# Optimization experiments

Hardware: AMD Instinct MI355X
Metric: run time of the kernel (lower is better)

## Reference

```python
import jax, jax.numpy as jnp
import numpy as np
from jax import lax

EPS = 1e-8


def setup_inputs() -> dict:
    key = jax.random.key(0)
    k1, k2, k3, k4 = jax.random.split(key, 4)
    B, C_in, C_out, K, S, H, W = 16, 64, 64, 3, 512, 256, 256
    x = jax.random.normal(k1, (B, C_in, H, W), dtype=jnp.float32)
    style = jax.random.normal(k2, (B, S), dtype=jnp.float32)
    # kaiming_normal fan_in linear: std = 1/sqrt(fan_in)
    mod_weight = jax.random.normal(k3, (C_in, S), dtype=jnp.float32) / np.sqrt(S)
    mod_bias = jnp.ones((C_in,), dtype=jnp.float32)  # init.constant_(bias, 1.0)
    weight = jax.random.normal(k4, (1, C_out, C_in, K, K), dtype=jnp.float32) / np.sqrt(C_in * K * K)
    return {"x": x, "style": style, "mod_weight": mod_weight,
            "mod_bias": mod_bias, "weight": weight}


def reference(x, style, mod_weight, mod_bias, weight):
    B, C, H, W = x.shape
    _, O, _, K, _ = weight.shape
    pad = K // 2
    # modulation: Linear(style) -> (B, C_in), broadcast over (O, kh, kw)
    s = style @ mod_weight.T + mod_bias                      # (B, C)
    w = weight * s[:, None, :, None, None]                   # (B, O, C, K, K)
    # demodulate
    demod = lax.rsqrt(jnp.sum(w * w, axis=(2, 3, 4), keepdims=True) + EPS)
    w = w * demod
    # grouped conv with groups = batch (per-sample weights)
    w = w.reshape(B * O, C, K, K)
    xg = x.reshape(1, B * C, H, W)
    out = lax.conv_general_dilated(
        xg, w,
        window_strides=(1, 1),
        padding=[(pad, pad), (pad, pad)],
        dimension_numbers=("NCHW", "OIHW", "NCHW"),
        feature_group_count=B,
    )
    return out.reshape(B, O, H, W)
```

## Files before the change

kernel.cpp:

```cpp
#include <hip/hip_runtime.h>

typedef _Float16 v8h __attribute__((ext_vector_type(8)));
typedef _Float16 v2h __attribute__((ext_vector_type(2)));
typedef float    v4f __attribute__((ext_vector_type(4)));
typedef unsigned int u32;

__global__ void style_kernel(const float* __restrict__ style,
                             const float* __restrict__ mw,
                             const float* __restrict__ mb,
                             float* __restrict__ s_out) {
    const int b = blockIdx.x;
    const int t = threadIdx.x;
    const int c = t >> 2, q = t & 3;
    const float* st = style + b * 512 + q * 128;
    const float* w  = mw + c * 512 + q * 128;
    float acc = 0.f;
    #pragma unroll 8
    for (int i = 0; i < 128; ++i) acc += st[i] * w[i];
    acc += __shfl_xor(acc, 1);
    acc += __shfl_xor(acc, 2);
    if (q == 0) s_out[b * 64 + c] = acc + mb[c];
}

__global__ void wprep_kernel(const float* __restrict__ weight,
                             const float* __restrict__ s,
                             _Float16* __restrict__ wA) {
    const int blk = blockIdx.x;
    const int b = blk >> 6, o = blk & 63;
    const int lane = threadIdx.x;
    const float* wo = weight + o * 576;
    const float* sb = s + b * 64;
    float vals[9];
    float sum = 0.f;
    #pragma unroll
    for (int k = 0; k < 9; ++k) {
        int e = lane + k * 64;
        int c = e / 9;
        float v = wo[e] * sb[c];
        vals[k] = v;
        sum += v * v;
    }
    #pragma unroll
    for (int off = 32; off; off >>= 1) sum += __shfl_xor(sum, off);
    const float demod = 1.f / sqrtf(sum + 1e-8f);
    #pragma unroll
    for (int k = 0; k < 9; ++k) {
        int e = lane + k * 64;
        int c = e / 9, tap = e - c * 9;
        int ks = c >> 5, lg = (c >> 3) & 3, j = c & 7;
        int dst = (((b * 9 + tap) * 8 + ks * 4 + (o >> 4)) * 64 + lg * 16 + (o & 15)) * 8 + j;
        wA[dst] = (_Float16)(vals[k] * demod);
    }
}

__global__ __launch_bounds__(256)
void xprep_kernel(const float* __restrict__ x, _Float16* __restrict__ xh) {
    __shared__ u32 lt[32 * 257];
    const int tid = threadIdx.x;
    const int h = blockIdx.x;
    const int b = blockIdx.y;

    const float* xr = x + ((size_t)b << 22) + (h << 8) + tid;
    float va[64];
    #pragma unroll
    for (int c = 0; c < 64; ++c)
        va[c] = __builtin_nontemporal_load(&xr[(size_t)c << 16]);
    #pragma unroll
    for (int cp = 0; cp < 32; ++cp) {
        union { v2h h2; u32 u; } pk;
        pk.h2[0] = (_Float16)va[2 * cp];
        pk.h2[1] = (_Float16)va[2 * cp + 1];
        lt[cp * 257 + tid] = pk.u;
    }

    if (tid < 5) {
        const int idx = blockIdx.x * 5 + tid;
        if (idx < 1028) {
            int row, col;
            if (idx < 258)        { row = 0;             col = idx; }
            else if (idx < 516)   { row = 257;           col = idx - 258; }
            else if (idx < 772)   { row = idx - 516 + 1; col = 0; }
            else                  { row = idx - 772 + 1; col = 257; }
            v8h z = {};
            _Float16* p = xh + (size_t)b * (258 * 258 * 64)
                             + (size_t)(row * 258 + col) * 64;
            #pragma unroll
            for (int g = 0; g < 8; ++g)
                *reinterpret_cast<v8h*>(p + g * 8) = z;
        }
    }
    __syncthreads();

    _Float16* rowb = xh + ((size_t)(b * 258 + h + 1) * 258 + 1) * 64;
    #pragma unroll
    for (int k = 0; k < 8; ++k) {
        const int G = (k << 8) + tid;
        const int pix = G >> 3, g = G & 7;
        union { u32 u[4]; v8h h8; } as_;
        #pragma unroll
        for (int jj = 0; jj < 4; ++jj)
            as_.u[jj] = lt[(4 * g + jj) * 257 + pix];
        *reinterpret_cast<v8h*>(rowb + (size_t)G * 8) = as_.h8;
    }
}

__global__ __launch_bounds__(256, 2)
void conv_kernel(const _Float16* __restrict__ xh,
                 const _Float16* __restrict__ wA,
                 float* __restrict__ out) {
    __shared__ __align__(16) _Float16 lds[612 * 64];

    const int tid = threadIdx.x;
    const int fid = blockIdx.x + (blockIdx.y << 3) + (blockIdx.z << 7);
    const int vid = ((fid & 7) << 8) + (fid >> 3);
    const int tx = vid & 7;
    const int ty = (vid >> 3) & 15;
    const int b  = vid >> 7;

    const int h0 = ty << 4;
    const int w0 = tx << 5;

    const int lane = tid & 63, wv = tid >> 6;
    const _Float16* xhb = xh + (size_t)b * (258 * 258 * 64);

    #pragma unroll
    for (int i = 0; i < 11; ++i) {
        const int k = wv + (i << 2);
        const int g0 = (k < 43) ? ((k << 6) < 2656 ? (k << 6) : 2656) : 0;
        const int A = g0 + lane;
        const int pix = A >> 3, g = A & 7;
        const int ph = pix / 34, pw = pix - ph * 34;
        const _Float16* src = xhb + (size_t)((h0 + ph) * 258 + (w0 + pw)) * 64
                                  + ((g ^ (pix & 7)) << 3);
        __builtin_amdgcn_global_load_lds(
            (const __attribute__((address_space(1))) void*)src,
            (__attribute__((address_space(3))) void*)(lds + (size_t)A * 8),
            16, 0, 0);
    }
    #pragma unroll
    for (int i = 0; i < 9; ++i) {
        const int k = wv + (i << 2);
        const int g0 = 2720 + ((k < 34) ? (k << 6) : 0);
        const int A = g0 + lane;
        const int pix = A >> 3, g = A & 7;
        const int ph = pix / 34, pw = pix - ph * 34;
        const _Float16* src = xhb + (size_t)((h0 + ph) * 258 + (w0 + pw)) * 64
                                  + ((g ^ (pix & 7)) << 3);
        __builtin_amdgcn_global_load_lds(
            (const __attribute__((address_space(1))) void*)src,
            (__attribute__((address_space(3))) void*)(lds + (size_t)A * 8),
            16, 0, 0);
    }

    const int n = lane & 15, lg = lane >> 4;
    const _Float16* wab = wA + (size_t)b * (9 * 8 * 64 * 8);

    v4f acc[4][2][2];

    asm volatile("s_waitcnt vmcnt(9)" ::: "memory");
    __builtin_amdgcn_s_barrier();
    __builtin_amdgcn_sched_barrier(0);

    #pragma unroll
    for (int ot = 0; ot < 4; ++ot)
        #pragma unroll
        for (int hf = 0; hf < 2; ++hf)
            #pragma unroll
            for (int rq = 0; rq < 2; ++rq)
                acc[ot][hf][rq] = (v4f)0.f;

    #pragma unroll
    for (int t = 0; t < 9; ++t) {
        const int dh = t / 3, dw = t - dh * 3;
        v8h a[4][2];
        #pragma unroll
        for (int ot = 0; ot < 4; ++ot)
            #pragma unroll
            for (int ks = 0; ks < 2; ++ks)
                a[ot][ks] = *reinterpret_cast<const v8h*>(
                    wab + ((size_t)((t * 8 + ks * 4 + ot) * 64 + lane)) * 8);
        #pragma unroll
        for (int rq = 0; rq < 2; ++rq) {
            const int R = wv + (rq << 2);
            #pragma unroll
            for (int hf = 0; hf < 2; ++hf) {
                const int pix = (R + dh) * 34 + n + (hf << 4) + dw;
                const char* pb = reinterpret_cast<const char*>(lds) + pix * 128;
                const int px7 = pix & 7;
                #pragma unroll
                for (int ks = 0; ks < 2; ++ks) {
                    v8h bf = *reinterpret_cast<const v8h*>(
                        pb + ((((ks << 2) + lg) ^ px7) << 4));
                    #pragma unroll
                    for (int ot = 0; ot < 4; ++ot)
                        acc[ot][hf][rq] = __builtin_amdgcn_mfma_f32_16x16x32_f16(
                            a[ot][ks], bf, acc[ot][hf][rq], 0, 0, 0);
                }
            }
        }
    }

    asm volatile("s_waitcnt vmcnt(0)" ::: "memory");
    __builtin_amdgcn_s_barrier();
    __builtin_amdgcn_sched_barrier(0);

    #pragma unroll
    for (int ot = 0; ot < 4; ++ot) {
        #pragma unroll
        for (int rq = 0; rq < 2; ++rq) {
            const int h = h0 + wv + (rq << 2);
            #pragma unroll
            for (int reg = 0; reg < 4; ++reg) {
                const int o = (ot << 4) + (lg << 2) + reg;
                float* op = out + (((size_t)(b * 64 + o)) << 16) + (h << 8) + w0 + n;
                __builtin_nontemporal_store(acc[ot][0][rq][reg], op);
                __builtin_nontemporal_store(acc[ot][1][rq][reg], op + 16);
            }
        }
    }

    #pragma unroll
    for (int ot = 0; ot < 4; ++ot)
        #pragma unroll
        for (int hf = 0; hf < 2; ++hf)
            #pragma unroll
            for (int rq = 0; rq < 2; ++rq)
                acc[ot][hf][rq] = (v4f)0.f;

    #pragma unroll
    for (int t = 0; t < 9; ++t) {
        const int dh = t / 3, dw = t - dh * 3;
        v8h a[4][2];
        #pragma unroll
        for (int ot = 0; ot < 4; ++ot)
            #pragma unroll
            for (int ks = 0; ks < 2; ++ks)
                a[ot][ks] = *reinterpret_cast<const v8h*>(
                    wab + ((size_t)((t * 8 + ks * 4 + ot) * 64 + lane)) * 8);
        #pragma unroll
        for (int rq = 0; rq < 2; ++rq) {
            const int R = wv + 8 + (rq << 2);
            #pragma unroll
            for (int hf = 0; hf < 2; ++hf) {
                const int pix = (R + dh) * 34 + n + (hf << 4) + dw;
                const char* pb = reinterpret_cast<const char*>(lds) + pix * 128;
                const int px7 = pix & 7;
                #pragma unroll
                for (int ks = 0; ks < 2; ++ks) {
                    v8h bf = *reinterpret_cast<const v8h*>(
                        pb + ((((ks << 2) + lg) ^ px7) << 4));
                    #pragma unroll
                    for (int ot = 0; ot < 4; ++ot)
                        acc[ot][hf][rq] = __builtin_amdgcn_mfma_f32_16x16x32_f16(
                            a[ot][ks], bf, acc[ot][hf][rq], 0, 0, 0);
                }
            }
        }
    }

    #pragma unroll
    for (int ot = 0; ot < 4; ++ot) {
        #pragma unroll
        for (int rq = 0; rq < 2; ++rq) {
            const int h = h0 + wv + 8 + (rq << 2);
            #pragma unroll
            for (int reg = 0; reg < 4; ++reg) {
                const int o = (ot << 4) + (lg << 2) + reg;
                float* op = out + (((size_t)(b * 64 + o)) << 16) + (h << 8) + w0 + n;
                __builtin_nontemporal_store(acc[ot][0][rq][reg], op);
                __builtin_nontemporal_store(acc[ot][1][rq][reg], op + 16);
            }
        }
    }
}

extern "C" void kernel_launch(void* const* d_in, const int* in_sizes, int n_in,
                              void* d_out, int out_size, void* d_ws, size_t ws_size,
                              hipStream_t stream) {
    const float* x      = (const float*)d_in[0];
    const float* style  = (const float*)d_in[1];
    const float* mw     = (const float*)d_in[2];
    const float* mb     = (const float*)d_in[3];
    const float* weight = (const float*)d_in[4];
    float* out = (float*)d_out;

    float*    s_ws = (float*)d_ws;
    _Float16* wA   = (_Float16*)((char*)d_ws + 4096);
    _Float16* xh   = (_Float16*)((char*)d_ws + 2u * 1024u * 1024u);

    style_kernel<<<16, 256, 0, stream>>>(style, mw, mb, s_ws);
    wprep_kernel<<<1024, 64, 0, stream>>>(weight, s_ws, wA);
    xprep_kernel<<<dim3(256, 16), 256, 0, stream>>>(x, xh);
    conv_kernel<<<dim3(8, 16, 16), 256, 0, stream>>>(xh, wA, out);
}
```

Baseline: 188.7 us.

## Shrink conv LDS tile to a 12-row ring buffer and raise occupancy to three blocks

The conv kernel now stages only the first 12 halo rows plus part of the rest into LDS, then refills the first rows with the remaining 6 rows after the first half's compute. The second half indexes rows modulo 12. This cuts LDS per block from 612 to 408 pixel slots, so the launch bound is raised to allow three resident blocks per CU. The trade-off is an extra barrier and a refill load in the middle of the kernel, plus a tighter register budget that could cause spills.

```diff
diff --git a/kernel.cpp b/kernel.cpp
--- a/kernel.cpp
+++ b/kernel.cpp
@@ -104,11 +104,11 @@
     }
 }
 
-__global__ __launch_bounds__(256, 2)
+__global__ __launch_bounds__(256, 3)
 void conv_kernel(const _Float16* __restrict__ xh,
                  const _Float16* __restrict__ wA,
                  float* __restrict__ out) {
-    __shared__ __align__(16) _Float16 lds[612 * 64];
+    __shared__ __align__(16) _Float16 lds[408 * 64];
 
     const int tid = threadIdx.x;
     const int fid = blockIdx.x + (blockIdx.y << 3) + (blockIdx.z << 7);
@@ -123,33 +123,28 @@
     const int lane = tid & 63, wv = tid >> 6;
     const _Float16* xhb = xh + (size_t)b * (258 * 258 * 64);
 
-    #pragma unroll
-    for (int i = 0; i < 11; ++i) {
-        const int k = wv + (i << 2);
-        const int g0 = (k < 43) ? ((k << 6) < 2656 ? (k << 6) : 2656) : 0;
-        const int A = g0 + lane;
-        const int pix = A >> 3, g = A & 7;
+    auto stage = [&](int Ag, int Ad) {
+        const int pix = Ag >> 3, g = Ag & 7;
         const int ph = pix / 34, pw = pix - ph * 34;
         const _Float16* src = xhb + (size_t)((h0 + ph) * 258 + (w0 + pw)) * 64
                                   + ((g ^ (pix & 7)) << 3);
         __builtin_amdgcn_global_load_lds(
             (const __attribute__((address_space(1))) void*)src,
-            (__attribute__((address_space(3))) void*)(lds + (size_t)A * 8),
+            (__attribute__((address_space(3))) void*)(lds + (size_t)Ad * 8),
             16, 0, 0);
-    }
-    #pragma unroll
-    for (int i = 0; i < 9; ++i) {
+    };
+
+    #pragma unroll
+    for (int i = 0; i < 11; ++i) {
         const int k = wv + (i << 2);
-        const int g0 = 2720 + ((k < 34) ? (k << 6) : 0);
-        const int A = g0 + lane;
-        const int pix = A >> 3, g = A & 7;
-        const int ph = pix / 34, pw = pix - ph * 34;
-        const _Float16* src = xhb + (size_t)((h0 + ph) * 258 + (w0 + pw)) * 64
-                                  + ((g ^ (pix & 7)) << 3);
-        __builtin_amdgcn_global_load_lds(
-            (const __attribute__((address_space(1))) void*)src,
-            (__attribute__((address_space(3))) void*)(lds + (size_t)A * 8),
-            16, 0, 0);
+        const int g0 = min(k << 6, 2656);
+        stage(g0 + lane, g0 + lane);
+    }
+    #pragma unroll
+    for (int i = 0; i < 3; ++i) {
+        const int k = wv + (i << 2);
+        const int g0 = 2720 + min(k << 6, 480);
+        stage(g0 + lane, g0 + lane);
     }
 
     const int n = lane & 15, lg = lane >> 4;
@@ -157,7 +152,7 @@
 
     v4f acc[4][2][2];
 
-    asm volatile("s_waitcnt vmcnt(9)" ::: "memory");
+    asm volatile("s_waitcnt vmcnt(3)" ::: "memory");
     __builtin_amdgcn_s_barrier();
     __builtin_amdgcn_sched_barrier(0);
 
@@ -200,6 +195,15 @@
         }
     }
 
+    __builtin_amdgcn_s_barrier();
+    __builtin_amdgcn_sched_barrier(0);
+
+    #pragma unroll
+    for (int i = 0; i < 7; ++i) {
+        const int k = wv + (i << 2);
+        const int g0 = min(k << 6, 1568);
+        stage(3264 + g0 + lane, g0 + lane);
+    }
     asm volatile("s_waitcnt vmcnt(0)" ::: "memory");
     __builtin_amdgcn_s_barrier();
     __builtin_amdgcn_sched_barrier(0);
@@ -239,12 +243,13 @@
                     wab + ((size_t)((t * 8 + ks * 4 + ot) * 64 + lane)) * 8);
         #pragma unroll
         for (int rq = 0; rq < 2; ++rq) {
-            const int R = wv + 8 + (rq << 2);
+            const int row = wv + 8 + (rq << 2) + dh;
+            const int srow = (row < 12) ? row : row - 12;
             #pragma unroll
             for (int hf = 0; hf < 2; ++hf) {
-                const int pix = (R + dh) * 34 + n + (hf << 4) + dw;
-                const char* pb = reinterpret_cast<const char*>(lds) + pix * 128;
-                const int px7 = pix & 7;
+                const int pixs = srow * 34 + n + (hf << 4) + dw;
+                const char* pb = reinterpret_cast<const char*>(lds) + pixs * 128;
+                const int px7 = pixs & 7;
                 #pragma unroll
                 for (int ks = 0; ks < 2; ++ks) {
                     v8h bf = *reinterpret_cast<const v8h*>(
```

Result: slower. 197.8 us (+4.8%).
